# Performance work log

Hardware: AMD Instinct MI355X
Metric: run time of the kernel (lower is better)

Reference implementation:

```python
import jax, jax.numpy as jnp
import numpy as np
from jax import lax

BN_EPS = 1e-3  # keras BatchNormalization default

def _conv(x, w):
    # x: (N,H,W,Cin), w: (kh,kw,Cin,Cout), 'same' padding, stride 1
    return lax.conv_general_dilated(x, w, (1, 1), 'SAME',
                                    dimension_numbers=('NHWC', 'HWIO', 'NHWC'))

def _hard_sigmoid(x):  # keras ConvLSTM2D default recurrent_activation
    return jnp.clip(0.2 * x + 0.5, 0.0, 1.0)

def _convlstm(x, Wx, Wh, b, return_sequences):
    # x: (B,T,H,W,Cin); Wx: (3,3,Cin,4F); Wh: (3,3,F,4F); gates order i,f,c,o
    B, T, H, W, Cin = x.shape
    F = Wh.shape[2]
    # precompute input-to-gate convs for all timesteps at once (one big conv)
    gx = _conv(x.reshape(B * T, H, W, Cin), Wx) + b
    gx = gx.reshape(B, T, H, W, 4 * F).transpose(1, 0, 2, 3, 4)  # (T,B,H,W,4F)
    h0 = jnp.zeros((B, H, W, F), x.dtype)
    c0 = jnp.zeros((B, H, W, F), x.dtype)

    def step(carry, gxt):
        h, c = carry
        z = gxt + _conv(h, Wh)
        zi, zf, zc, zo = jnp.split(z, 4, axis=-1)
        c = _hard_sigmoid(zf) * c + _hard_sigmoid(zi) * jnp.tanh(zc)
        h = _hard_sigmoid(zo) * jnp.tanh(c)
        return (h, c), h

    (hT, _), hs = lax.scan(step, (h0, c0), gx)
    if return_sequences:
        return hs.transpose(1, 0, 2, 3, 4)  # (B,T,H,W,F)
    return hT  # (B,H,W,F)

def _bn(x, gamma, beta, mean, var):
    return (x - mean) * (gamma * lax.rsqrt(var + BN_EPS)) + beta

def _pool_thw(x):  # MaxPool3D(pool_size=(1,2,2))
    B, T, H, W, C = x.shape
    return x.reshape(B, T, H // 2, 2, W // 2, 2, C).max(axis=(3, 5))

def _pool_hw(x):  # MaxPool2D()
    B, H, W, C = x.shape
    return x.reshape(B, H // 2, 2, W // 2, 2, C).max(axis=(2, 4))

def setup_inputs() -> dict:
    key = jax.random.key(0)
    ks = jax.random.split(key, 16)
    s = 0.05  # weight scale
    d = {
        'x':   jax.random.normal(ks[0], (8, 12, 64, 64, 3), jnp.float32),
        'W1x': jax.random.normal(ks[1], (3, 3, 3, 64), jnp.float32) * s,
        'W1h': jax.random.normal(ks[2], (3, 3, 16, 64), jnp.float32) * s,
        'b1':  jnp.zeros((64,), jnp.float32),
        'g1':  jnp.ones((16,), jnp.float32),
        'be1': jnp.zeros((16,), jnp.float32),
        'm1':  jax.random.normal(ks[3], (16,), jnp.float32) * 0.1,
        'v1':  jax.random.uniform(ks[4], (16,), jnp.float32) + 0.5,
        'W2x': jax.random.normal(ks[5], (3, 3, 16, 128), jnp.float32) * s,
        'W2h': jax.random.normal(ks[6], (3, 3, 32, 128), jnp.float32) * s,
        'b2':  jnp.zeros((128,), jnp.float32),
        'g2':  jnp.ones((32,), jnp.float32),
        'be2': jnp.zeros((32,), jnp.float32),
        'm2':  jax.random.normal(ks[7], (32,), jnp.float32) * 0.1,
        'v2':  jax.random.uniform(ks[8], (32,), jnp.float32) + 0.5,
        'W3x': jax.random.normal(ks[9], (3, 3, 32, 256), jnp.float32) * s,
        'W3h': jax.random.normal(ks[10], (3, 3, 64, 256), jnp.float32) * s,
        'b3':  jnp.zeros((256,), jnp.float32),
        'Wd1': jax.random.normal(ks[11], (4096, 10000), jnp.float32) * 0.01,
        'bd1': jnp.zeros((10000,), jnp.float32),
        'Wd2': jax.random.normal(ks[12], (10000, 1000), jnp.float32) * 0.01,
        'bd2': jnp.zeros((1000,), jnp.float32),
        'Wd3': jax.random.normal(ks[13], (1000, 100), jnp.float32) * 0.03,
        'bd3': jnp.zeros((100,), jnp.float32),
        'Wd4': jax.random.normal(ks[14], (100, 10), jnp.float32) * 0.1,
        'bd4': jnp.zeros((10,), jnp.float32),
        'Wc':  jax.random.normal(ks[15], (10, 1), jnp.float32) * 0.3,
        'bc':  jnp.zeros((1,), jnp.float32),
    }
    return d

def reference(x, W1x, W1h, b1, g1, be1, m1, v1,
              W2x, W2h, b2, g2, be2, m2, v2,
              W3x, W3h, b3,
              Wd1, bd1, Wd2, bd2, Wd3, bd3, Wd4, bd4, Wc, bc):
    h = _convlstm(x, W1x, W1h, b1, True)          # (B,12,64,64,16)
    h = _bn(h, g1, be1, m1, v1)
    h = _pool_thw(h)                              # (B,12,32,32,16)
    h = _convlstm(h, W2x, W2h, b2, True)          # (B,12,32,32,32)
    h = _bn(h, g2, be2, m2, v2)
    h = _pool_thw(h)                              # (B,12,16,16,32)
    h = _convlstm(h, W3x, W3h, b3, False)         # (B,16,16,64)
    h = _pool_hw(h)                               # (B,8,8,64)
    h = h.reshape(h.shape[0], -1)                 # (B,4096)
    h = h @ Wd1 + bd1
    h = h @ Wd2 + bd2
    h = h @ Wd3 + bd3
    h = h @ Wd4 + bd4
    return h @ Wc + bc                            # (B,1)
```

## Files before the change

### kernel.cpp

```cpp
#include <hip/hip_runtime.h>
#include <hip/hip_bf16.h>
#include <math.h>

template<int H, int W, int Cin, int Cout, int TH, int TW, int COL, int NG>
__global__ __launch_bounds__(256) void conv3x3_bias(
    const float* __restrict__ in, const float* __restrict__ wt,
    const float* __restrict__ bias, float* __restrict__ out)
{
  static_assert(COL * NG == Cout, "cout coverage");
  constexpr int CIN_P = (Cin % 4 == 0) ? Cin : ((Cin + 3) / 4) * 4;
  constexpr int TILES_X = W / TW, TILES_Y = H / TH;
  constexpr int PAD_W = TW + 2, PAD_H = TH + 2;
  constexpr int LDS_N = PAD_H * PAD_W * CIN_P;
  constexpr int NPG = 256 / COL;
  constexpr int PPT = TH * TW / NPG;
  __shared__ __align__(16) float tile[LDS_N];

  int blk = blockIdx.x;
  int n = blk / (TILES_X * TILES_Y);
  int trem = blk % (TILES_X * TILES_Y);
  int ty = trem / TILES_X, tx = trem % TILES_X;
  int y0 = ty * TH, x0 = tx * TW;
  const float* inN = in + (size_t)n * H * W * Cin;

  for (int i = threadIdx.x; i < LDS_N; i += 256) {
    int ci = i % CIN_P; int rem = i / CIN_P;
    int xx = rem % PAD_W; int yy = rem / PAD_W;
    int gy = y0 + yy - 1, gx = x0 + xx - 1;
    float v = 0.f;
    if (ci < Cin && gy >= 0 && gy < H && gx >= 0 && gx < W)
      v = inN[((size_t)gy * W + gx) * Cin + ci];
    tile[i] = v;
  }
  __syncthreads();

  int cobase = threadIdx.x % COL;
  int pg = threadIdx.x / COL;
  float* outN = out + (size_t)n * H * W * Cout;

  float acc[NG][PPT];
#pragma unroll
  for (int g = 0; g < NG; ++g) {
    float bco = bias[g * COL + cobase];
#pragma unroll
    for (int j = 0; j < PPT; ++j) acc[g][j] = bco;
  }

#pragma unroll
  for (int kh = 0; kh < 3; ++kh)
#pragma unroll
  for (int kw = 0; kw < 3; ++kw) {
    const float* wtap = wt + ((size_t)(kh * 3 + kw) * Cin) * Cout + cobase;
#pragma unroll 1
    for (int c4 = 0; c4 < CIN_P; c4 += 4) {
      float w[NG][4];
#pragma unroll
      for (int g = 0; g < NG; ++g)
#pragma unroll
        for (int ch = 0; ch < 4; ++ch) {
          w[g][ch] = (Cin % 4 == 0 || c4 + ch < Cin)
                         ? wtap[(size_t)(c4 + ch) * Cout + g * COL] : 0.f;
        }
#pragma unroll
      for (int j = 0; j < PPT; ++j) {
        int p = pg * PPT + j;
        int ly = p / TW, lx = p % TW;
        const float4 h4 = *(const float4*)&tile[((ly + kh) * PAD_W + (lx + kw)) * CIN_P + c4];
#pragma unroll
        for (int g = 0; g < NG; ++g)
          acc[g][j] += h4.x * w[g][0] + h4.y * w[g][1] + h4.z * w[g][2] + h4.w * w[g][3];
      }
    }
  }

#pragma unroll
  for (int j = 0; j < PPT; ++j) {
    int p = pg * PPT + j;
    int ly = p / TW, lx = p % TW;
    float* op = &outN[((size_t)(y0 + ly) * W + (x0 + lx)) * Cout + cobase];
#pragma unroll
    for (int g = 0; g < NG; ++g) op[g * COL] = acc[g][j];
  }
}

__device__ __forceinline__ float hsig(float x) {
  return fminf(fmaxf(0.2f * x + 0.5f, 0.f), 1.f);
}

template<int H, int W, int F, int TH, int TW>
__global__ __launch_bounds__(256) void lstm_step(
    const float* __restrict__ gx, long gx_bstride,
    const float* __restrict__ hprev, long hp_bstride,
    const float* __restrict__ wh,
    float* __restrict__ c,
    float* __restrict__ hout, long ho_bstride,
    int first)
{
  constexpr int TILES_X = W / TW, TILES_Y = H / TH;
  constexpr int PAD_W = TW + 2, PAD_H = TH + 2;
  constexpr int LDS_N = PAD_H * PAD_W * F;
  __shared__ __align__(16) float tile[LDS_N];

  int blk = blockIdx.x;
  int b = blk / (TILES_X * TILES_Y);
  int trem = blk % (TILES_X * TILES_Y);
  int ty = trem / TILES_X, tx = trem % TILES_X;
  int y0 = ty * TH, x0 = tx * TW;

  if (first) {
    for (int i = threadIdx.x; i < LDS_N; i += 256) tile[i] = 0.f;
  } else {
    const float* hb = hprev + (size_t)b * hp_bstride;
    for (int i = threadIdx.x; i < LDS_N; i += 256) {
      int ci = i % F; int rem = i / F;
      int xx = rem % PAD_W, yy = rem / PAD_W;
      int gy = y0 + yy - 1, gxp = x0 + xx - 1;
      float v = 0.f;
      if (gy >= 0 && gy < H && gxp >= 0 && gxp < W)
        v = hb[((size_t)gy * W + gxp) * F + ci];
      tile[i] = v;
    }
  }
  __syncthreads();

  constexpr int G = 256 / F;
  constexpr int P = TH * TW;
  constexpr int NP = P / G;
  int f = threadIdx.x % F;
  int pg = threadIdx.x / F;

  float acc[4][NP];
  const float* gxb = gx + (size_t)b * gx_bstride;
#pragma unroll
  for (int j = 0; j < NP; ++j) {
    int p = pg * NP + j;
    int gy = y0 + p / TW, gxp = x0 + p % TW;
    size_t base = ((size_t)gy * W + gxp) * 4 * F;
#pragma unroll
    for (int g = 0; g < 4; ++g) acc[g][j] = gxb[base + g * F + f];
  }

#pragma unroll
  for (int kh = 0; kh < 3; ++kh)
#pragma unroll
  for (int kw = 0; kw < 3; ++kw) {
    const float* wtap = wh + ((size_t)(kh * 3 + kw) * F) * 4 * F + f;
#pragma unroll 1
    for (int c4 = 0; c4 < F; c4 += 4) {
      float4 h4[NP];
#pragma unroll
      for (int j = 0; j < NP; ++j) {
        int p = pg * NP + j;
        int ly = p / TW, lx = p % TW;
        h4[j] = *(const float4*)&tile[((ly + kh) * PAD_W + (lx + kw)) * F + c4];
      }
      const float* wc0 = wtap + (size_t)c4 * 4 * F;
#pragma unroll
      for (int g = 0; g < 4; ++g) {
        float w0 = wc0[(size_t)g * F];
        float w1 = wc0[(size_t)4 * F + g * F];
        float w2 = wc0[(size_t)8 * F + g * F];
        float w3 = wc0[(size_t)12 * F + g * F];
#pragma unroll
        for (int j = 0; j < NP; ++j)
          acc[g][j] += h4[j].x * w0 + h4[j].y * w1 + h4[j].z * w2 + h4[j].w * w3;
      }
    }
  }

  float* cb = c + (size_t)b * H * W * F;
  float* hb2 = hout + (size_t)b * ho_bstride;
#pragma unroll
  for (int j = 0; j < NP; ++j) {
    int p = pg * NP + j;
    int gy = y0 + p / TW, gxp = x0 + p % TW;
    size_t idx = ((size_t)gy * W + gxp) * F + f;
    float zi = acc[0][j], zf = acc[1][j], zc = acc[2][j], zo = acc[3][j];
    float cold = first ? 0.f : cb[idx];
    float cn = hsig(zf) * cold + hsig(zi) * tanhf(zc);
    cb[idx] = cn;
    hb2[idx] = hsig(zo) * tanhf(cn);
  }
}

__global__ void bnpool_kernel(const float* __restrict__ in,
                              const float* __restrict__ g, const float* __restrict__ be,
                              const float* __restrict__ m, const float* __restrict__ v,
                              float* __restrict__ out, int total, int H, int W, int F)
{
  int i = blockIdx.x * 256 + threadIdx.x;
  if (i >= total) return;
  int f = i % F; int rem = i / F;
  int x = rem % (W / 2); rem /= (W / 2);
  int y = rem % (H / 2); int nt = rem / (H / 2);
  float scale = g[f] * rsqrtf(v[f] + 1e-3f);
  float shift = be[f] - m[f] * scale;
  const float* base = in + (((size_t)nt * H + 2 * y) * W + 2 * x) * F + f;
  float a0 = base[0] * scale + shift;
  float a1 = base[F] * scale + shift;
  float a2 = base[(size_t)W * F] * scale + shift;
  float a3 = base[(size_t)W * F + F] * scale + shift;
  out[i] = fmaxf(fmaxf(a0, a1), fmaxf(a2, a3));
}

__global__ void poolhw_kernel(const float* __restrict__ in, float* __restrict__ out, int total)
{
  int i = blockIdx.x * 256 + threadIdx.x;
  if (i >= total) return;
  int f = i % 64; int rem = i / 64;
  int x = rem % 8; rem /= 8;
  int y = rem % 8; int b = rem / 8;
  const float* base = in + (((size_t)b * 16 + 2 * y) * 16 + 2 * x) * 64 + f;
  float a0 = base[0], a1 = base[64], a2 = base[16 * 64], a3 = base[16 * 64 + 64];
  out[i] = fmaxf(fmaxf(a0, a1), fmaxf(a2, a3));
}

__global__ __launch_bounds__(256) void dense_partial(
    const float* __restrict__ x, const float* __restrict__ w,
    float* __restrict__ part, int K, int N, int kchunk)
{
  extern __shared__ __align__(16) float xs[];
  int kb = blockIdx.y;
  int k0 = kb * kchunk;
  int klen = min(kchunk, K - k0);
  for (int i = threadIdx.x; i < klen * 8; i += 256) {
    int kk = i >> 3, b = i & 7;
    xs[i] = x[(size_t)b * K + k0 + kk];
  }
  __syncthreads();
  int co = blockIdx.x * 256 + threadIdx.x;
  if (co >= N) return;
  float acc[8];
#pragma unroll
  for (int b = 0; b < 8; ++b) acc[b] = 0.f;
  const float4* xs4 = (const float4*)xs;
  const float* wp = w + (size_t)k0 * N + co;
#pragma unroll 4
  for (int kk = 0; kk < klen; ++kk) {
    float wv = wp[(size_t)kk * N];
    float4 lo = xs4[kk * 2], hi = xs4[kk * 2 + 1];
    acc[0] += lo.x * wv; acc[1] += lo.y * wv;
    acc[2] += lo.z * wv; acc[3] += lo.w * wv;
    acc[4] += hi.x * wv; acc[5] += hi.y * wv;
    acc[6] += hi.z * wv; acc[7] += hi.w * wv;
  }
#pragma unroll
  for (int b = 0; b < 8; ++b)
    part[((size_t)kb * 8 + b) * N + co] = acc[b];
}

__global__ __launch_bounds__(256) void dense_reduce(
    const float* __restrict__ part, const float* __restrict__ bias,
    float* __restrict__ out, int N, int S)
{
  int co = blockIdx.x * 256 + threadIdx.x;
  int b = blockIdx.y;
  if (co >= N) return;
  float acc = bias[co];
#pragma unroll 4
  for (int kb = 0; kb < S; ++kb)
    acc += part[((size_t)kb * 8 + b) * N + co];
  out[(size_t)b * N + co] = acc;
}

__global__ void dense_part(const float* __restrict__ x, const float* __restrict__ w,
                           const float* __restrict__ bias, float* __restrict__ out,
                           int K, int N, int kchunk)
{
  extern __shared__ float xs[];
  int co = blockIdx.x * 256 + threadIdx.x;
  int kb = blockIdx.y;
  int k0 = kb * kchunk;
  int k1 = min(k0 + kchunk, K);
  int klen = k1 - k0;
  for (int i = threadIdx.x; i < klen * 8; i += 256) {
    int b = i / klen; int kk = i % klen;
    xs[b * kchunk + kk] = x[(size_t)b * K + k0 + kk];
  }
  __syncthreads();
  if (co >= N) return;
  float acc[8];
#pragma unroll
  for (int b = 0; b < 8; ++b) acc[b] = 0.f;
#pragma unroll 1
  for (int k = k0; k < k1; ++k) {
    float wv = w[(size_t)k * N + co];
    int kk = k - k0;
#pragma unroll
    for (int b = 0; b < 8; ++b) acc[b] += xs[b * kchunk + kk] * wv;
  }
  float bi = (kb == 0) ? bias[co] : 0.f;
#pragma unroll
  for (int b = 0; b < 8; ++b) atomicAdd(&out[(size_t)b * N + co], acc[b] + bi);
}

__global__ void dense_tail(const float* __restrict__ d3,
                           const float* __restrict__ w4, const float* __restrict__ b4,
                           const float* __restrict__ wc, const float* __restrict__ bc,
                           float* __restrict__ out)
{
  __shared__ float d4[8][10];
  int t = threadIdx.x;
  if (t < 80) {
    int b = t / 10, co = t % 10;
    float acc = b4[co];
    for (int k = 0; k < 100; ++k) acc += d3[b * 100 + k] * w4[k * 10 + co];
    d4[b][co] = acc;
  }
  __syncthreads();
  if (t < 8) {
    float acc = bc[0];
    for (int j = 0; j < 10; ++j) acc += d4[t][j] * wc[j];
    out[t] = acc;
  }
}

extern "C" void kernel_launch(void* const* d_in, const int* in_sizes, int n_in,
                              void* d_out, int out_size, void* d_ws, size_t ws_size,
                              hipStream_t stream)
{
  const float* x   = (const float*)d_in[0];
  const float* W1x = (const float*)d_in[1];
  const float* W1h = (const float*)d_in[2];
  const float* b1  = (const float*)d_in[3];
  const float* g1  = (const float*)d_in[4];
  const float* be1 = (const float*)d_in[5];
  const float* m1  = (const float*)d_in[6];
  const float* v1  = (const float*)d_in[7];
  const float* W2x = (const float*)d_in[8];
  const float* W2h = (const float*)d_in[9];
  const float* b2  = (const float*)d_in[10];
  const float* g2  = (const float*)d_in[11];
  const float* be2 = (const float*)d_in[12];
  const float* m2  = (const float*)d_in[13];
  const float* v2  = (const float*)d_in[14];
  const float* W3x = (const float*)d_in[15];
  const float* W3h = (const float*)d_in[16];
  const float* b3  = (const float*)d_in[17];
  const float* Wd1 = (const float*)d_in[18];
  const float* bd1 = (const float*)d_in[19];
  const float* Wd2 = (const float*)d_in[20];
  const float* bd2 = (const float*)d_in[21];
  const float* Wd3 = (const float*)d_in[22];
  const float* bd3 = (const float*)d_in[23];
  const float* Wd4 = (const float*)d_in[24];
  const float* bd4 = (const float*)d_in[25];
  const float* Wc  = (const float*)d_in[26];
  const float* bc  = (const float*)d_in[27];

  char* ws = (char*)d_ws;
  size_t off = 0;
  auto alloc = [&](size_t bytes) { size_t r = off; off = (off + bytes + 255) & ~(size_t)255; return r; };
  size_t oR0   = alloc(100663296);
  size_t oR1   = alloc(25165824);
  size_t oR2   = alloc(6291456);
  size_t oR3   = alloc(2097152);
  size_t oh3a  = alloc(524288);
  size_t oh3b  = alloc(524288);
  size_t oflat = alloc(131072);
  size_t od1   = alloc(320000);
  size_t od2   = alloc(32000);
  size_t od3   = alloc(3200);
  (void)ws_size; (void)in_sizes; (void)n_in; (void)out_size;

  float* gx1   = (float*)(ws + oR0);
  float* gx2   = (float*)(ws + oR0);
  float* gx3   = (float*)(ws + oR0);
  float* part1 = (float*)(ws + oR0);
  float* part2 = (float*)(ws + oR0 + 33554432);
  float* hseq1 = (float*)(ws + oR1);
  float* hseq2 = (float*)(ws + oR1);
  float* pool1 = (float*)(ws + oR2);
  float* pool2 = (float*)(ws + oR2);
  float* cbuf  = (float*)(ws + oR3);
  float* h3a   = (float*)(ws + oh3a);
  float* h3b   = (float*)(ws + oh3b);
  float* flat  = (float*)(ws + oflat);
  float* d1    = (float*)(ws + od1);
  float* d2    = (float*)(ws + od2);
  float* d3b   = (float*)(ws + od3);

  const int B = 8, T = 12;

  conv3x3_bias<64, 64, 3, 64, 4, 8, 32, 2><<<96 * 128, 256, 0, stream>>>(x, W1x, b1, gx1);
  {
    const long gxs = (long)T * 64 * 64 * 64;
    const long hs  = (long)T * 64 * 64 * 16;
    for (int t = 0; t < T; ++t) {
      lstm_step<64, 64, 16, 4, 8><<<B * 128, 256, 0, stream>>>(
          gx1 + (size_t)t * 64 * 64 * 64, gxs,
          t ? hseq1 + (size_t)(t - 1) * 64 * 64 * 16 : nullptr, hs,
          W1h, cbuf, hseq1 + (size_t)t * 64 * 64 * 16, hs, t == 0);
    }
  }
  {
    int total = B * T * 32 * 32 * 16;
    bnpool_kernel<<<(total + 255) / 256, 256, 0, stream>>>(hseq1, g1, be1, m1, v1, pool1, total, 64, 64, 16);
  }

  conv3x3_bias<32, 32, 16, 128, 4, 8, 32, 4><<<96 * 32, 256, 0, stream>>>(pool1, W2x, b2, gx2);
  {
    const long gxs = (long)T * 32 * 32 * 128;
    const long hs  = (long)T * 32 * 32 * 32;
    for (int t = 0; t < T; ++t) {
      lstm_step<32, 32, 32, 4, 4><<<B * 64, 256, 0, stream>>>(
          gx2 + (size_t)t * 32 * 32 * 128, gxs,
          t ? hseq2 + (size_t)(t - 1) * 32 * 32 * 32 : nullptr, hs,
          W2h, cbuf, hseq2 + (size_t)t * 32 * 32 * 32, hs, t == 0);
    }
  }
  {
    int total = B * T * 16 * 16 * 32;
    bnpool_kernel<<<(total + 255) / 256, 256, 0, stream>>>(hseq2, g2, be2, m2, v2, pool2, total, 32, 32, 32);
  }

  conv3x3_bias<16, 16, 32, 256, 4, 8, 64, 4><<<96 * 8, 256, 0, stream>>>(pool2, W3x, b3, gx3);
  {
    const long gxs = (long)T * 16 * 16 * 256;
    const long hs  = (long)16 * 16 * 64;
    for (int t = 0; t < T; ++t) {
      float* hout = (t % 2 == 0) ? h3a : h3b;
      const float* hp = (t % 2 == 0) ? h3b : h3a;
      lstm_step<16, 16, 64, 2, 2><<<B * 64, 256, 0, stream>>>(
          gx3 + (size_t)t * 16 * 16 * 256, gxs,
          t ? hp : nullptr, hs,
          W3h, cbuf, hout, hs, t == 0);
    }
  }
  poolhw_kernel<<<(32768 + 255) / 256, 256, 0, stream>>>(h3b, flat, 32768);

  dense_partial<<<dim3(40, 64), 256, 64 * 8 * 4, stream>>>(flat, Wd1, part1, 4096, 10000, 64);
  dense_reduce<<<dim3(40, 8), 256, 0, stream>>>(part1, bd1, d1, 10000, 64);
  dense_partial<<<dim3(4, 125), 256, 80 * 8 * 4, stream>>>(d1, Wd2, part2, 10000, 1000, 80);
  dense_reduce<<<dim3(4, 8), 256, 0, stream>>>(part2, bd2, d2, 1000, 125);
  hipMemsetAsync(d3b, 0, 3200, stream);
  dense_part<<<dim3(1, 8), 256, 8 * 128 * 4, stream>>>(d2, Wd3, bd3, d3b, 1000, 100, 128);
  dense_tail<<<1, 128, 0, stream>>>(d3b, Wd4, bd4, Wc, bc, (float*)d_out);
}
```

Measured before the change: 1.640 ms.

## Pre-transpose conv weights for float4 loads, retile LSTM steps, simplify dense3

Adds small kernels that rearrange the input and recurrent conv weights so each thread reads its four input-channel weights as one contiguous float4 instead of four strided scalar loads. It also changes the tile shapes for the layer-1 and layer-3 LSTM step kernels (larger tiles, fewer blocks), and replaces the atomic-based third dense layer plus its memset with a simple per-output kernel. The aim is to cut scattered weight-load traffic and instruction count in the conv loops, at the cost of extra launches to rewrite the weights on every call. The transposed layout also makes each thread touch a different cache line, so loads that were coalesced across a wavefront are no longer coalesced.

New measurement: 2.833 ms. 72.7% more time.

```diff
diff --git a/kernel.cpp b/kernel.cpp
--- a/kernel.cpp
+++ b/kernel.cpp
@@ -2,9 +2,31 @@
 #include <hip/hip_bf16.h>
 #include <math.h>
 
+__global__ void transpose_wx(const float* __restrict__ src, float* __restrict__ dst,
+                             int Cin, int CinP, int Cout)
+{
+  int i = blockIdx.x * 256 + threadIdx.x;
+  int total = 9 * Cout * CinP;
+  if (i >= total) return;
+  int c = i % CinP; int rem = i / CinP;
+  int co = rem % Cout; int tap = rem / Cout;
+  dst[i] = (c < Cin) ? src[((size_t)tap * Cin + c) * Cout + co] : 0.f;
+}
+
+__global__ void transpose_wh(const float* __restrict__ src, float* __restrict__ dst, int F)
+{
+  int i = blockIdx.x * 256 + threadIdx.x;
+  int total = 9 * 4 * F * F;
+  if (i >= total) return;
+  int c = i % F; int rem = i / F;
+  int f = rem % F; rem /= F;
+  int g = rem % 4; int tap = rem / 4;
+  dst[i] = src[((size_t)tap * F + c) * 4 * F + g * F + f];
+}
+
 template<int H, int W, int Cin, int Cout, int TH, int TW, int COL, int NG>
 __global__ __launch_bounds__(256) void conv3x3_bias(
-    const float* __restrict__ in, const float* __restrict__ wt,
+    const float* __restrict__ in, const float* __restrict__ wtT,
     const float* __restrict__ bias, float* __restrict__ out)
 {
   static_assert(COL * NG == Cout, "cout coverage");
@@ -50,17 +72,13 @@
   for (int kh = 0; kh < 3; ++kh)
 #pragma unroll
   for (int kw = 0; kw < 3; ++kw) {
-    const float* wtap = wt + ((size_t)(kh * 3 + kw) * Cin) * Cout + cobase;
+    const float* wtap = wtT + (size_t)(kh * 3 + kw) * Cout * CIN_P;
 #pragma unroll 1
     for (int c4 = 0; c4 < CIN_P; c4 += 4) {
-      float w[NG][4];
+      float4 w[NG];
 #pragma unroll
       for (int g = 0; g < NG; ++g)
-#pragma unroll
-        for (int ch = 0; ch < 4; ++ch) {
-          w[g][ch] = (Cin % 4 == 0 || c4 + ch < Cin)
-                         ? wtap[(size_t)(c4 + ch) * Cout + g * COL] : 0.f;
-        }
+        w[g] = *(const float4*)&wtap[(size_t)(g * COL + cobase) * CIN_P + c4];
 #pragma unroll
       for (int j = 0; j < PPT; ++j) {
         int p = pg * PPT + j;
@@ -68,7 +86,7 @@
         const float4 h4 = *(const float4*)&tile[((ly + kh) * PAD_W + (lx + kw)) * CIN_P + c4];
 #pragma unroll
         for (int g = 0; g < NG; ++g)
-          acc[g][j] += h4.x * w[g][0] + h4.y * w[g][1] + h4.z * w[g][2] + h4.w * w[g][3];
+          acc[g][j] += h4.x * w[g].x + h4.y * w[g].y + h4.z * w[g].z + h4.w * w[g].w;
       }
     }
   }
@@ -91,7 +109,7 @@
 __global__ __launch_bounds__(256) void lstm_step(
     const float* __restrict__ gx, long gx_bstride,
     const float* __restrict__ hprev, long hp_bstride,
-    const float* __restrict__ wh,
+    const float* __restrict__ whT,
     float* __restrict__ c,
     float* __restrict__ hout, long ho_bstride,
     int first)
@@ -144,7 +162,10 @@
   for (int kh = 0; kh < 3; ++kh)
 #pragma unroll
   for (int kw = 0; kw < 3; ++kw) {
-    const float* wtap = wh + ((size_t)(kh * 3 + kw) * F) * 4 * F + f;
+    const float* w0p = whT + ((size_t)((kh * 3 + kw) * 4 + 0) * F + f) * F;
+    const float* w1p = whT + ((size_t)((kh * 3 + kw) * 4 + 1) * F + f) * F;
+    const float* w2p = whT + ((size_t)((kh * 3 + kw) * 4 + 2) * F + f) * F;
+    const float* w3p = whT + ((size_t)((kh * 3 + kw) * 4 + 3) * F + f) * F;
 #pragma unroll 1
     for (int c4 = 0; c4 < F; c4 += 4) {
       float4 h4[NP];
@@ -154,16 +175,16 @@
         int ly = p / TW, lx = p % TW;
         h4[j] = *(const float4*)&tile[((ly + kh) * PAD_W + (lx + kw)) * F + c4];
       }
-      const float* wc0 = wtap + (size_t)c4 * 4 * F;
-#pragma unroll
-      for (int g = 0; g < 4; ++g) {
-        float w0 = wc0[(size_t)g * F];
-        float w1 = wc0[(size_t)4 * F + g * F];
-        float w2 = wc0[(size_t)8 * F + g * F];
-        float w3 = wc0[(size_t)12 * F + g * F];
-#pragma unroll
-        for (int j = 0; j < NP; ++j)
-          acc[g][j] += h4[j].x * w0 + h4[j].y * w1 + h4[j].z * w2 + h4[j].w * w3;
+      float4 w0 = *(const float4*)&w0p[c4];
+      float4 w1 = *(const float4*)&w1p[c4];
+      float4 w2 = *(const float4*)&w2p[c4];
+      float4 w3 = *(const float4*)&w3p[c4];
+#pragma unroll
+      for (int j = 0; j < NP; ++j) {
+        acc[0][j] += h4[j].x * w0.x + h4[j].y * w0.y + h4[j].z * w0.z + h4[j].w * w0.w;
+        acc[1][j] += h4[j].x * w1.x + h4[j].y * w1.y + h4[j].z * w1.z + h4[j].w * w1.w;
+        acc[2][j] += h4[j].x * w2.x + h4[j].y * w2.y + h4[j].z * w2.z + h4[j].w * w2.w;
+        acc[3][j] += h4[j].x * w3.x + h4[j].y * w3.y + h4[j].z * w3.z + h4[j].w * w3.w;
       }
     }
   }
@@ -263,35 +284,18 @@
   out[(size_t)b * N + co] = acc;
 }
 
-__global__ void dense_part(const float* __restrict__ x, const float* __restrict__ w,
-                           const float* __restrict__ bias, float* __restrict__ out,
-                           int K, int N, int kchunk)
-{
-  extern __shared__ float xs[];
-  int co = blockIdx.x * 256 + threadIdx.x;
-  int kb = blockIdx.y;
-  int k0 = kb * kchunk;
-  int k1 = min(k0 + kchunk, K);
-  int klen = k1 - k0;
-  for (int i = threadIdx.x; i < klen * 8; i += 256) {
-    int b = i / klen; int kk = i % klen;
-    xs[b * kchunk + kk] = x[(size_t)b * K + k0 + kk];
-  }
-  __syncthreads();
-  if (co >= N) return;
-  float acc[8];
-#pragma unroll
-  for (int b = 0; b < 8; ++b) acc[b] = 0.f;
-#pragma unroll 1
-  for (int k = k0; k < k1; ++k) {
-    float wv = w[(size_t)k * N + co];
-    int kk = k - k0;
-#pragma unroll
-    for (int b = 0; b < 8; ++b) acc[b] += xs[b * kchunk + kk] * wv;
-  }
-  float bi = (kb == 0) ? bias[co] : 0.f;
-#pragma unroll
-  for (int b = 0; b < 8; ++b) atomicAdd(&out[(size_t)b * N + co], acc[b] + bi);
+__global__ void dense_small(const float* __restrict__ x, const float* __restrict__ w,
+                            const float* __restrict__ bias, float* __restrict__ out,
+                            int K, int N, int total)
+{
+  int idx = blockIdx.x * 256 + threadIdx.x;
+  if (idx >= total) return;
+  int b = idx / N, co = idx % N;
+  float acc = bias[co];
+  const float* xb = x + (size_t)b * K;
+#pragma unroll 4
+  for (int k = 0; k < K; ++k) acc += xb[k] * w[(size_t)k * N + co];
+  out[idx] = acc;
 }
 
 __global__ void dense_tail(const float* __restrict__ d3,
@@ -351,16 +355,22 @@
   char* ws = (char*)d_ws;
   size_t off = 0;
   auto alloc = [&](size_t bytes) { size_t r = off; off = (off + bytes + 255) & ~(size_t)255; return r; };
-  size_t oR0   = alloc(100663296);
-  size_t oR1   = alloc(25165824);
-  size_t oR2   = alloc(6291456);
-  size_t oR3   = alloc(2097152);
-  size_t oh3a  = alloc(524288);
-  size_t oh3b  = alloc(524288);
-  size_t oflat = alloc(131072);
-  size_t od1   = alloc(320000);
-  size_t od2   = alloc(32000);
-  size_t od3   = alloc(3200);
+  size_t oR0    = alloc(100663296);
+  size_t oR1    = alloc(25165824);
+  size_t oR2    = alloc(6291456);
+  size_t oR3    = alloc(2097152);
+  size_t oh3a   = alloc(524288);
+  size_t oh3b   = alloc(524288);
+  size_t oflat  = alloc(131072);
+  size_t od1    = alloc(320000);
+  size_t od2    = alloc(32000);
+  size_t od3    = alloc(3200);
+  size_t oWx1T  = alloc(9216);
+  size_t oWx2T  = alloc(73728);
+  size_t oWx3T  = alloc(294912);
+  size_t oWh1T  = alloc(36864);
+  size_t oWh2T  = alloc(147456);
+  size_t oWh3T  = alloc(589824);
   (void)ws_size; (void)in_sizes; (void)n_in; (void)out_size;
 
   float* gx1   = (float*)(ws + oR0);
@@ -379,18 +389,31 @@
   float* d1    = (float*)(ws + od1);
   float* d2    = (float*)(ws + od2);
   float* d3b   = (float*)(ws + od3);
+  float* Wx1T  = (float*)(ws + oWx1T);
+  float* Wx2T  = (float*)(ws + oWx2T);
+  float* Wx3T  = (float*)(ws + oWx3T);
+  float* Wh1T  = (float*)(ws + oWh1T);
+  float* Wh2T  = (float*)(ws + oWh2T);
+  float* Wh3T  = (float*)(ws + oWh3T);
 
   const int B = 8, T = 12;
 
-  conv3x3_bias<64, 64, 3, 64, 4, 8, 32, 2><<<96 * 128, 256, 0, stream>>>(x, W1x, b1, gx1);
+  transpose_wx<<<(9 * 64 * 4 + 255) / 256, 256, 0, stream>>>(W1x, Wx1T, 3, 4, 64);
+  transpose_wx<<<(9 * 128 * 16 + 255) / 256, 256, 0, stream>>>(W2x, Wx2T, 16, 16, 128);
+  transpose_wx<<<(9 * 256 * 32 + 255) / 256, 256, 0, stream>>>(W3x, Wx3T, 32, 32, 256);
+  transpose_wh<<<(9 * 4 * 16 * 16 + 255) / 256, 256, 0, stream>>>(W1h, Wh1T, 16);
+  transpose_wh<<<(9 * 4 * 32 * 32 + 255) / 256, 256, 0, stream>>>(W2h, Wh2T, 32);
+  transpose_wh<<<(9 * 4 * 64 * 64 + 255) / 256, 256, 0, stream>>>(W3h, Wh3T, 64);
+
+  conv3x3_bias<64, 64, 3, 64, 4, 8, 32, 2><<<96 * 128, 256, 0, stream>>>(x, Wx1T, b1, gx1);
   {
     const long gxs = (long)T * 64 * 64 * 64;
     const long hs  = (long)T * 64 * 64 * 16;
     for (int t = 0; t < T; ++t) {
-      lstm_step<64, 64, 16, 4, 8><<<B * 128, 256, 0, stream>>>(
+      lstm_step<64, 64, 16, 8, 8><<<B * 64, 256, 0, stream>>>(
           gx1 + (size_t)t * 64 * 64 * 64, gxs,
           t ? hseq1 + (size_t)(t - 1) * 64 * 64 * 16 : nullptr, hs,
-          W1h, cbuf, hseq1 + (size_t)t * 64 * 64 * 16, hs, t == 0);
+          Wh1T, cbuf, hseq1 + (size_t)t * 64 * 64 * 16, hs, t == 0);
     }
   }
   {
@@ -398,7 +421,7 @@
     bnpool_kernel<<<(total + 255) / 256, 256, 0, stream>>>(hseq1, g1, be1, m1, v1, pool1, total, 64, 64, 16);
   }
 
-  conv3x3_bias<32, 32, 16, 128, 4, 8, 32, 4><<<96 * 32, 256, 0, stream>>>(pool1, W2x, b2, gx2);
+  conv3x3_bias<32, 32, 16, 128, 4, 8, 32, 4><<<96 * 32, 256, 0, stream>>>(pool1, Wx2T, b2, gx2);
   {
     const long gxs = (long)T * 32 * 32 * 128;
     const long hs  = (long)T * 32 * 32 * 32;
@@ -406,7 +429,7 @@
       lstm_step<32, 32, 32, 4, 4><<<B * 64, 256, 0, stream>>>(
           gx2 + (size_t)t * 32 * 32 * 128, gxs,
           t ? hseq2 + (size_t)(t - 1) * 32 * 32 * 32 : nullptr, hs,
-          W2h, cbuf, hseq2 + (size_t)t * 32 * 32 * 32, hs, t == 0);
+          Wh2T, cbuf, hseq2 + (size_t)t * 32 * 32 * 32, hs, t == 0);
     }
   }
   {
@@ -414,17 +437,17 @@
     bnpool_kernel<<<(total + 255) / 256, 256, 0, stream>>>(hseq2, g2, be2, m2, v2, pool2, total, 32, 32, 32);
   }
 
-  conv3x3_bias<16, 16, 32, 256, 4, 8, 64, 4><<<96 * 8, 256, 0, stream>>>(pool2, W3x, b3, gx3);
+  conv3x3_bias<16, 16, 32, 256, 4, 8, 64, 4><<<96 * 8, 256, 0, stream>>>(pool2, Wx3T, b3, gx3);
   {
     const long gxs = (long)T * 16 * 16 * 256;
     const long hs  = (long)16 * 16 * 64;
     for (int t = 0; t < T; ++t) {
       float* hout = (t % 2 == 0) ? h3a : h3b;
       const float* hp = (t % 2 == 0) ? h3b : h3a;
-      lstm_step<16, 16, 64, 2, 2><<<B * 64, 256, 0, stream>>>(
+      lstm_step<16, 16, 64, 2, 4><<<B * 32, 256, 0, stream>>>(
           gx3 + (size_t)t * 16 * 16 * 256, gxs,
           t ? hp : nullptr, hs,
-          W3h, cbuf, hout, hs, t == 0);
+          Wh3T, cbuf, hout, hs, t == 0);
     }
   }
   poolhw_kernel<<<(32768 + 255) / 256, 256, 0, stream>>>(h3b, flat, 32768);
@@ -433,7 +456,6 @@
   dense_reduce<<<dim3(40, 8), 256, 0, stream>>>(part1, bd1, d1, 10000, 64);
   dense_partial<<<dim3(4, 125), 256, 80 * 8 * 4, stream>>>(d1, Wd2, part2, 10000, 1000, 80);
   dense_reduce<<<dim3(4, 8), 256, 0, stream>>>(part2, bd2, d2, 1000, 125);
-  hipMemsetAsync(d3b, 0, 3200, stream);
-  dense_part<<<dim3(1, 8), 256, 8 * 128 * 4, stream>>>(d2, Wd3, bd3, d3b, 1000, 100, 128);
+  dense_small<<<(800 + 255) / 256, 256, 0, stream>>>(d2, Wd3, bd3, d3b, 1000, 100, 800);
   dense_tail<<<1, 128, 0, stream>>>(d3b, Wd4, bd4, Wc, bc, (float*)d_out);
 }
```
